# Kernel tuning notes

Hardware: AMD Instinct MI355X
Metric: run time of the kernel (lower is better)

The kernel has to match this reference:

```python
import jax, jax.numpy as jnp
import numpy as np

N_NODES = 100_000
N_EDGES = 3_200_000
WEIGHT_LIMIT = 5000.0
RIDGE = 1e-7


def _polynomial_basis(diff):
    # diff: [E, 2] -> [E, 5] basis (x, y, x*y, x^2, y^2)
    x = diff[:, 0]
    y = diff[:, 1]
    return jnp.stack([x, y, x * y, x * x, y * y], axis=-1)


def setup_inputs() -> dict:
    key = jax.random.key(0)
    k1, k2, k3 = jax.random.split(key, 3)
    pos = jax.random.normal(k1, (N_NODES, 2), dtype=jnp.float32)
    row = jax.random.randint(k2, (N_EDGES,), 0, N_NODES, dtype=jnp.int64)
    col = jax.random.randint(k3, (N_EDGES,), 0, N_NODES, dtype=jnp.int64)
    edge_index = jnp.stack([row, col], axis=0)
    return {"pos": pos, "edge_index": edge_index}


def reference(pos, edge_index):
    # With a dense random graph, 2-hop extension adds no edges, so the
    # augmented edge_index equals the original edge_index.
    row = edge_index[0]
    col = edge_index[1]
    n = pos.shape[0]

    # Edge displacement (detached in the original module).
    diff = jax.lax.stop_gradient(pos[col] - pos[row])  # [E, 2]
    H = _polynomial_basis(diff).astype(jnp.float32)    # [E, 5]

    # Per-edge outer products, scatter-accumulated per source node.
    M_edge = H[:, :, None] * H[:, None, :]                          # [E, 5, 5]
    M_node = jax.ops.segment_sum(M_edge, row, num_segments=n)      # [N, 5, 5]
    M_node = M_node + RIDGE * jnp.eye(5, dtype=jnp.float32)

    # Laplacian RHS: [0, 0, 0, 2, 2] per node (coefficients of x^2, y^2).
    L = jnp.zeros((n, 5), dtype=jnp.float32).at[:, 3:].set(2.0)

    # C = M^{-1} L (per-node 5x5 solve).
    C = jnp.linalg.solve(M_node, L[..., None])[..., 0]              # [N, 5]

    # Per-edge Laplacian weights.
    weights = jnp.sum(C[row] * H, axis=1)                           # [E]
    return jnp.clip(weights, -WEIGHT_LIMIT, WEIGHT_LIMIT)
```

## Files before the change

### kernel.cpp

```cpp
#include <hip/hip_runtime.h>
#include <math.h>

constexpr float WLIM = 5000.0f;
constexpr double RIDGE = 1e-7;

#define G 256
#define MAXNB 1024
#define BN 128
#define CAP 5120
#define EBUF_CAP 12544

__global__ __launch_bounds__(1024) void k_sort(const int* __restrict__ row,
                                               const int* __restrict__ col,
                                               int* __restrict__ table,
                                               unsigned int* __restrict__ sorted,
                                               int nE, int CE, int NB) {
    __shared__ int h[MAXNB];
    __shared__ int t[MAXNB];
    __shared__ unsigned int ebuf[EBUF_CAP];
    const int g = blockIdx.x, tid = threadIdx.x;
    const int s = g * CE;
    const int e_end = min(s + CE, nE);
    const int cnt = e_end - s;

    for (int i = tid; i < MAXNB; i += 1024) h[i] = 0;
    __syncthreads();
    for (int i = s + tid; i < e_end; i += 1024)
        atomicAdd(&h[row[i] >> 7], 1);
    __syncthreads();
    int v = h[tid];
    t[tid] = v;
    __syncthreads();
    for (int d = 1; d < MAXNB; d <<= 1) {
        int u = (tid >= d) ? t[tid - d] : 0;
        __syncthreads();
        t[tid] += u;
        __syncthreads();
    }
    int excl = t[tid] - v;
    if (tid < NB) {
        table[(size_t)tid * G + g] = excl;
        h[tid] = excl;
    }
    if (tid == 0) table[(size_t)NB * G + g] = cnt;
    __syncthreads();
    for (int i = s + tid; i < e_end; i += 1024) {
        int r = row[i];
        int c = col[i];
        int b = r >> 7;
        int p = atomicAdd(&h[b], 1);
        ebuf[p] = ((unsigned)(r & 127) << 17) | (unsigned)c;
    }
    __syncthreads();
    for (int i = tid; i < cnt; i += 1024)
        sorted[s + i] = ebuf[i];
}

__global__ __launch_bounds__(256) void k_node3(const float2* __restrict__ pos,
                                               const unsigned int* __restrict__ sorted,
                                               const int* __restrict__ table,
                                               float* __restrict__ rec,
                                               int nN, int CE, int NB) {
    __shared__ unsigned int ebuf[CAP];
    __shared__ int off[BN + 1];
    __shared__ int cur[BN];
    __shared__ int goff0[G], glen[G];
    const int b = blockIdx.x, tid = threadIdx.x;

    int off0 = table[(size_t)b * G + tid];
    int off1 = table[(size_t)(b + 1) * G + tid];
    int len = off1 - off0;
    goff0[tid] = off0; glen[tid] = len;
    if (tid < BN + 1) off[tid] = 0;
    __syncthreads();

    const int gbase = tid * CE + off0;
    for (int j = 0; j < len; ++j)
        atomicAdd(&off[(sorted[gbase + j] >> 17) + 1], 1);
    __syncthreads();
    if (tid == 0) {
        int a = 0;
        for (int i = 0; i <= BN; ++i) { a += off[i]; off[i] = a; }
    }
    __syncthreads();
    const int total = off[BN];
    if (tid < BN) cur[tid] = off[tid];
    __syncthreads();

    const bool fits = (total <= CAP);
    if (fits) {
        for (int j = 0; j < len; ++j) {
            unsigned v = sorted[gbase + j];
            int p = atomicAdd(&cur[(int)(v >> 17)], 1);
            ebuf[p] = v & 0x1FFFFu;
        }
    }
    __syncthreads();

    const int node = tid >> 1;
    const int half = tid & 1;
    const int n = (b << 7) + node;
    float m[15];
    #pragma unroll
    for (int i = 0; i < 15; ++i) m[i] = 0.0f;
    float2 pr = make_float2(0.f, 0.f);
    if (n < nN) {
        pr = pos[n];
        if (fits) {
            int j0 = off[node], j1 = off[node + 1];
            for (int j = j0 + half; j < j1; j += 2) {
                float2 pc = pos[ebuf[j]];
                float x = pc.x - pr.x;
                float y = pc.y - pr.y;
                float xy = x * y, xx = x * x, yy = y * y;
                m[0]  += x * x;   m[1]  += x * y;   m[2]  += x * xy;  m[3]  += x * xx;  m[4]  += x * yy;
                m[5]  += y * y;   m[6]  += y * xy;  m[7]  += y * xx;  m[8]  += y * yy;
                m[9]  += xy * xy; m[10] += xy * xx; m[11] += xy * yy;
                m[12] += xx * xx; m[13] += xx * yy;
                m[14] += yy * yy;
            }
        } else {
            for (int g2 = half; g2 < G; g2 += 2) {
                int base2 = g2 * CE + goff0[g2];
                for (int j = 0; j < glen[g2]; ++j) {
                    unsigned v = sorted[base2 + j];
                    if ((int)(v >> 17) == node) {
                        float2 pc = pos[v & 0x1FFFFu];
                        float x = pc.x - pr.x;
                        float y = pc.y - pr.y;
                        float xy = x * y, xx = x * x, yy = y * y;
                        m[0]  += x * x;   m[1]  += x * y;   m[2]  += x * xy;  m[3]  += x * xx;  m[4]  += x * yy;
                        m[5]  += y * y;   m[6]  += y * xy;  m[7]  += y * xx;  m[8]  += y * yy;
                        m[9]  += xy * xy; m[10] += xy * xx; m[11] += xy * yy;
                        m[12] += xx * xx; m[13] += xx * yy;
                        m[14] += yy * yy;
                    }
                }
            }
        }
    }
    #pragma unroll
    for (int i = 0; i < 15; ++i) m[i] += __shfl_xor(m[i], 1);

    if (half == 0 && n < nN) {
        double A[5][5];
        {
            int idx = 0;
            #pragma unroll
            for (int i = 0; i < 5; ++i) {
                #pragma unroll
                for (int j = i; j < 5; ++j) {
                    double vv = (double)m[idx++];
                    A[i][j] = vv;
                    A[j][i] = vv;
                }
            }
        }
        #pragma unroll
        for (int i = 0; i < 5; ++i) A[i][i] += RIDGE;

        #pragma unroll
        for (int k = 0; k < 5; ++k) {
            double d = A[k][k];
            d = sqrt(fmax(d, 1e-300));
            A[k][k] = d;
            double inv = 1.0 / d;
            #pragma unroll
            for (int i = k + 1; i < 5; ++i) A[i][k] *= inv;
            #pragma unroll
            for (int j = k + 1; j < 5; ++j) {
                #pragma unroll
                for (int i = j; i < 5; ++i) A[i][j] -= A[i][k] * A[j][k];
            }
        }
        double bb[5] = {0.0, 0.0, 0.0, 2.0, 2.0};
        double y[5];
        #pragma unroll
        for (int i = 0; i < 5; ++i) {
            double sv = bb[i];
            #pragma unroll
            for (int k = 0; k < 5; ++k) {
                if (k < i) sv -= A[i][k] * y[k];
            }
            y[i] = sv / A[i][i];
        }
        double xs[5];
        #pragma unroll
        for (int ii = 4; ii >= 0; --ii) {
            double sv = y[ii];
            #pragma unroll
            for (int k = 0; k < 5; ++k) {
                if (k > ii) sv -= A[k][ii] * xs[k];
            }
            xs[ii] = sv / A[ii][ii];
        }
        float4* rb = (float4*)(rec + (size_t)n * 8);
        rb[0] = make_float4((float)xs[0], (float)xs[1], (float)xs[2], (float)xs[3]);
        rb[1] = make_float4((float)xs[4], pr.x, pr.y, 0.0f);
    }
}

__global__ __launch_bounds__(256) void k_weights(const float2* __restrict__ pos,
                                                 const int* __restrict__ row,
                                                 const int* __restrict__ col,
                                                 const float* __restrict__ rec,
                                                 float* __restrict__ out,
                                                 int nE) {
    int e = blockIdx.x * blockDim.x + threadIdx.x;
    if (e >= nE) return;
    int r = row[e];
    int c = col[e];
    const float4* rb = (const float4*)(rec + (size_t)r * 8);
    float4 r0 = rb[0];
    float4 r1 = rb[1];
    float2 pc = pos[c];
    float x = pc.x - r1.y;
    float y = pc.y - r1.z;
    float w = r0.x * x + r0.y * y + r0.z * (x * y) + r0.w * (x * x) + r1.x * (y * y);
    w = fminf(fmaxf(w, -WLIM), WLIM);
    out[e] = w;
}

extern "C" void kernel_launch(void* const* d_in, const int* in_sizes, int n_in,
                              void* d_out, int out_size, void* d_ws, size_t ws_size,
                              hipStream_t stream) {
    const float2* pos = (const float2*)d_in[0];
    const int* ei = (const int*)d_in[1];
    const int nN = in_sizes[0] / 2;
    const int nE = in_sizes[1] / 2;
    const int* row = ei;
    const int* col = ei + nE;

    const int NB = (nN + BN - 1) >> 7;
    const int CE = (nE + G - 1) / G;

    int* table = (int*)d_ws;
    size_t roff = (((size_t)(NB + 1) * G) + 3) & ~(size_t)3;
    float* rec = (float*)((int*)d_ws + roff);

    unsigned int* sorted = (unsigned int*)d_out;
    float* out = (float*)d_out;

    k_sort<<<G, 1024, 0, stream>>>(row, col, table, sorted, nE, CE, NB);
    k_node3<<<NB, 256, 0, stream>>>(pos, sorted, table, rec, nN, CE, NB);
    k_weights<<<(nE + 255) / 256, 256, 0, stream>>>(pos, row, col, rec, out, nE);
}
```

Before: 92.52 us.

## Vectorize edge loads/stores and replace shared-memory scans with wavefront shuffle scans

Row/col reads in the bucket sort and weight kernels now use int4 loads, and the sorted buffer and output are written with 128-bit stores. The barrier-heavy Hillis-Steele prefix sum in k_sort and the serial single-thread scan in k_node3 are replaced by two-level wavefront shuffle scans. This is meant to cut memory instruction count and synchronization overhead. The tail paths add some code complexity and depend on alignment checks (CE divisible by 4).

```diff
diff --git a/kernel.cpp b/kernel.cpp
--- a/kernel.cpp
+++ b/kernel.cpp
@@ -16,44 +16,96 @@
                                                unsigned int* __restrict__ sorted,
                                                int nE, int CE, int NB) {
     __shared__ int h[MAXNB];
-    __shared__ int t[MAXNB];
+    __shared__ int wt[16];
     __shared__ unsigned int ebuf[EBUF_CAP];
     const int g = blockIdx.x, tid = threadIdx.x;
+    const int lane = tid & 63, wid = tid >> 6;
     const int s = g * CE;
     const int e_end = min(s + CE, nE);
     const int cnt = e_end - s;
+    const bool vec = ((CE & 3) == 0);
 
     for (int i = tid; i < MAXNB; i += 1024) h[i] = 0;
     __syncthreads();
-    for (int i = s + tid; i < e_end; i += 1024)
-        atomicAdd(&h[row[i] >> 7], 1);
+    if (vec) {
+        const int4* r4p = (const int4*)(row + s);
+        int nv = cnt >> 2;
+        for (int i = tid; i < nv; i += 1024) {
+            int4 r4 = r4p[i];
+            atomicAdd(&h[r4.x >> 7], 1);
+            atomicAdd(&h[r4.y >> 7], 1);
+            atomicAdd(&h[r4.z >> 7], 1);
+            atomicAdd(&h[r4.w >> 7], 1);
+        }
+        for (int i = (nv << 2) + tid; i < cnt; i += 1024)
+            atomicAdd(&h[row[s + i] >> 7], 1);
+    } else {
+        for (int i = s + tid; i < e_end; i += 1024)
+            atomicAdd(&h[row[i] >> 7], 1);
+    }
     __syncthreads();
     int v = h[tid];
-    t[tid] = v;
-    __syncthreads();
-    for (int d = 1; d < MAXNB; d <<= 1) {
-        int u = (tid >= d) ? t[tid - d] : 0;
-        __syncthreads();
-        t[tid] += u;
-        __syncthreads();
-    }
-    int excl = t[tid] - v;
+    int x = v;
+    #pragma unroll
+    for (int d = 1; d < 64; d <<= 1) {
+        int u = __shfl_up(x, d);
+        if (lane >= d) x += u;
+    }
+    if (lane == 63) wt[wid] = x;
+    __syncthreads();
+    if (tid < 16) {
+        int w = wt[tid];
+        int xx = w;
+        #pragma unroll
+        for (int d = 1; d < 16; d <<= 1) {
+            int u = __shfl_up(xx, d);
+            if (tid >= d) xx += u;
+        }
+        wt[tid] = xx - w;
+    }
+    __syncthreads();
+    int excl = (x - v) + wt[wid];
     if (tid < NB) {
         table[(size_t)tid * G + g] = excl;
         h[tid] = excl;
     }
     if (tid == 0) table[(size_t)NB * G + g] = cnt;
     __syncthreads();
-    for (int i = s + tid; i < e_end; i += 1024) {
-        int r = row[i];
-        int c = col[i];
-        int b = r >> 7;
-        int p = atomicAdd(&h[b], 1);
-        ebuf[p] = ((unsigned)(r & 127) << 17) | (unsigned)c;
-    }
-    __syncthreads();
-    for (int i = tid; i < cnt; i += 1024)
-        sorted[s + i] = ebuf[i];
+    if (vec) {
+        const int4* r4p = (const int4*)(row + s);
+        const int4* c4p = (const int4*)(col + s);
+        int nv = cnt >> 2;
+        for (int i = tid; i < nv; i += 1024) {
+            int4 r4 = r4p[i];
+            int4 c4 = c4p[i];
+            int p;
+            p = atomicAdd(&h[r4.x >> 7], 1); ebuf[p] = ((unsigned)(r4.x & 127) << 17) | (unsigned)c4.x;
+            p = atomicAdd(&h[r4.y >> 7], 1); ebuf[p] = ((unsigned)(r4.y & 127) << 17) | (unsigned)c4.y;
+            p = atomicAdd(&h[r4.z >> 7], 1); ebuf[p] = ((unsigned)(r4.z & 127) << 17) | (unsigned)c4.z;
+            p = atomicAdd(&h[r4.w >> 7], 1); ebuf[p] = ((unsigned)(r4.w & 127) << 17) | (unsigned)c4.w;
+        }
+        for (int i = (nv << 2) + tid; i < cnt; i += 1024) {
+            int r = row[s + i], c = col[s + i];
+            int p = atomicAdd(&h[r >> 7], 1);
+            ebuf[p] = ((unsigned)(r & 127) << 17) | (unsigned)c;
+        }
+    } else {
+        for (int i = s + tid; i < e_end; i += 1024) {
+            int r = row[i], c = col[i];
+            int p = atomicAdd(&h[r >> 7], 1);
+            ebuf[p] = ((unsigned)(r & 127) << 17) | (unsigned)c;
+        }
+    }
+    __syncthreads();
+    if (vec) {
+        uint4* dst = (uint4*)(sorted + s);
+        const uint4* src = (const uint4*)ebuf;
+        int nv = cnt >> 2;
+        for (int i = tid; i < nv; i += 1024) dst[i] = src[i];
+        for (int i = (nv << 2) + tid; i < cnt; i += 1024) sorted[s + i] = ebuf[i];
+    } else {
+        for (int i = tid; i < cnt; i += 1024) sorted[s + i] = ebuf[i];
+    }
 }
 
 __global__ __launch_bounds__(256) void k_node3(const float2* __restrict__ pos,
@@ -62,30 +114,44 @@
                                                float* __restrict__ rec,
                                                int nN, int CE, int NB) {
     __shared__ unsigned int ebuf[CAP];
+    __shared__ int cnt[BN];
     __shared__ int off[BN + 1];
     __shared__ int cur[BN];
     __shared__ int goff0[G], glen[G];
+    __shared__ int wt2[2];
     const int b = blockIdx.x, tid = threadIdx.x;
 
     int off0 = table[(size_t)b * G + tid];
     int off1 = table[(size_t)(b + 1) * G + tid];
     int len = off1 - off0;
     goff0[tid] = off0; glen[tid] = len;
-    if (tid < BN + 1) off[tid] = 0;
+    if (tid < BN) cnt[tid] = 0;
     __syncthreads();
 
     const int gbase = tid * CE + off0;
     for (int j = 0; j < len; ++j)
-        atomicAdd(&off[(sorted[gbase + j] >> 17) + 1], 1);
-    __syncthreads();
-    if (tid == 0) {
-        int a = 0;
-        for (int i = 0; i <= BN; ++i) { a += off[i]; off[i] = a; }
+        atomicAdd(&cnt[sorted[gbase + j] >> 17], 1);
+    __syncthreads();
+    int sv = 0, sx = 0;
+    if (tid < BN) {
+        sv = cnt[tid];
+        sx = sv;
+        #pragma unroll
+        for (int d = 1; d < 64; d <<= 1) {
+            int u = __shfl_up(sx, d);
+            if ((tid & 63) >= d) sx += u;
+        }
+        if ((tid & 63) == 63) wt2[tid >> 6] = sx;
+    }
+    __syncthreads();
+    if (tid < BN) {
+        int incl = sx + ((tid >> 6) ? wt2[0] : 0);
+        off[tid] = incl - sv;
+        cur[tid] = incl - sv;
+        if (tid == BN - 1) off[BN] = incl;
     }
     __syncthreads();
     const int total = off[BN];
-    if (tid < BN) cur[tid] = off[tid];
-    __syncthreads();
 
     const bool fits = (total <= CAP);
     if (fits) {
@@ -177,22 +243,22 @@
         double y[5];
         #pragma unroll
         for (int i = 0; i < 5; ++i) {
-            double sv = bb[i];
+            double sv2 = bb[i];
             #pragma unroll
             for (int k = 0; k < 5; ++k) {
-                if (k < i) sv -= A[i][k] * y[k];
-            }
-            y[i] = sv / A[i][i];
+                if (k < i) sv2 -= A[i][k] * y[k];
+            }
+            y[i] = sv2 / A[i][i];
         }
         double xs[5];
         #pragma unroll
         for (int ii = 4; ii >= 0; --ii) {
-            double sv = y[ii];
+            double sv2 = y[ii];
             #pragma unroll
             for (int k = 0; k < 5; ++k) {
-                if (k > ii) sv -= A[k][ii] * xs[k];
-            }
-            xs[ii] = sv / A[ii][ii];
+                if (k > ii) sv2 -= A[k][ii] * xs[k];
+            }
+            xs[ii] = sv2 / A[ii][ii];
         }
         float4* rb = (float4*)(rec + (size_t)n * 8);
         rb[0] = make_float4((float)xs[0], (float)xs[1], (float)xs[2], (float)xs[3]);
@@ -205,20 +271,42 @@
                                                  const int* __restrict__ col,
                                                  const float* __restrict__ rec,
                                                  float* __restrict__ out,
-                                                 int nE) {
-    int e = blockIdx.x * blockDim.x + threadIdx.x;
-    if (e >= nE) return;
-    int r = row[e];
-    int c = col[e];
-    const float4* rb = (const float4*)(rec + (size_t)r * 8);
-    float4 r0 = rb[0];
-    float4 r1 = rb[1];
-    float2 pc = pos[c];
-    float x = pc.x - r1.y;
-    float y = pc.y - r1.z;
-    float w = r0.x * x + r0.y * y + r0.z * (x * y) + r0.w * (x * x) + r1.x * (y * y);
-    w = fminf(fmaxf(w, -WLIM), WLIM);
-    out[e] = w;
+                                                 int nE4, int nE) {
+    int t = blockIdx.x * blockDim.x + threadIdx.x;
+    if (t < nE4) {
+        int4 r4 = ((const int4*)row)[t];
+        int4 c4 = ((const int4*)col)[t];
+        float4 o;
+        #pragma unroll
+        for (int k = 0; k < 4; ++k) {
+            int r = (k == 0) ? r4.x : (k == 1) ? r4.y : (k == 2) ? r4.z : r4.w;
+            int c = (k == 0) ? c4.x : (k == 1) ? c4.y : (k == 2) ? c4.z : c4.w;
+            const float4* rb = (const float4*)(rec + (size_t)r * 8);
+            float4 q0 = rb[0];
+            float4 q1 = rb[1];
+            float2 pc = pos[c];
+            float x = pc.x - q1.y;
+            float y = pc.y - q1.z;
+            float w = q0.x * x + q0.y * y + q0.z * (x * y) + q0.w * (x * x) + q1.x * (y * y);
+            w = fminf(fmaxf(w, -WLIM), WLIM);
+            if (k == 0) o.x = w; else if (k == 1) o.y = w; else if (k == 2) o.z = w; else o.w = w;
+        }
+        ((float4*)out)[t] = o;
+    }
+    int tail0 = nE4 * 4;
+    int i = tail0 + t;
+    if (t < (nE - tail0)) {
+        int r = row[i];
+        int c = col[i];
+        const float4* rb = (const float4*)(rec + (size_t)r * 8);
+        float4 q0 = rb[0];
+        float4 q1 = rb[1];
+        float2 pc = pos[c];
+        float x = pc.x - q1.y;
+        float y = pc.y - q1.z;
+        float w = q0.x * x + q0.y * y + q0.z * (x * y) + q0.w * (x * x) + q1.x * (y * y);
+        out[i] = fminf(fmaxf(w, -WLIM), WLIM);
+    }
 }
 
 extern "C" void kernel_launch(void* const* d_in, const int* in_sizes, int n_in,
@@ -241,7 +329,8 @@
     unsigned int* sorted = (unsigned int*)d_out;
     float* out = (float*)d_out;
 
+    const int nE4 = nE / 4;
     k_sort<<<G, 1024, 0, stream>>>(row, col, table, sorted, nE, CE, NB);
     k_node3<<<NB, 256, 0, stream>>>(pos, sorted, table, rec, nN, CE, NB);
-    k_weights<<<(nE + 255) / 256, 256, 0, stream>>>(pos, row, col, rec, out, nE);
+    k_weights<<<(nE4 + 255) / 256, 256, 0, stream>>>(pos, row, col, rec, out, nE4, nE);
 }
```

Result: slower. 96.53 us (+4.3%).
